# Kernel optimization log

Hardware: AMD Instinct MI355X
Metric: run time of the kernel (lower is better)

Reference implementation:

```python
import jax, jax.numpy as jnp
import numpy as np

F4_E2M1_MAX = 6.0
F8E4M3_MAX = 448.0
E4M3_EPS = 0.015625  # torch.finfo(float8_e4m3fn).tiny = 2**-6
BLOCK = 16
KE2M1 = jnp.array([0.0, 0.5, 1.0, 1.5, 2.0, 3.0, 4.0, 6.0], dtype=jnp.float32)


def round_to_e4m3(x):
    # emulate cast to float8_e4m3fn and back (round-to-nearest-even)
    return x.astype(jnp.float8_e4m3fn).astype(jnp.float32)


def fp4_121_positive(x):
    step1 = jnp.round(2.0 * x) / 2.0   # subnormal-ish region [0,2): step 0.5
    step2 = jnp.round(x)               # [2,4): step 1
    step3 = 2.0 * jnp.round(x / 2.0)   # [4,6]: step 2
    return jnp.where(x < 2.0, step1, jnp.where(x < 4.0, step2, step3))


def cast_to_fp4(x):
    return jnp.sign(x) * fp4_121_positive(jnp.abs(x))


def unpack_fp4_from_uint8(a, m, n):
    # a: int-typed tensor holding byte values in [0,256); two fp4 codes per byte
    high = (a.reshape(-1) >> 4) & 0xF
    low = a.reshape(-1) & 0xF
    combined = jnp.stack((low, high), axis=1).reshape(m, n)  # interleave low,high
    signs = (combined & 8) != 0
    abs_idx = combined & 7
    return KE2M1[abs_idx] * jnp.where(signs, -1.0, 1.0)


def dequant_nvfp4_packed(data_lp, out_scales, per_tensor_scale):
    m, half_n = data_lp.shape
    n = half_n * 2
    data_hp = unpack_fp4_from_uint8(data_lp, m, n)           # [m, n] float32
    scale_fp = out_scales / per_tensor_scale                  # [m, n/16]
    data_hp = data_hp.reshape(m, -1, BLOCK) * scale_fp.reshape(m, -1, 1)
    return data_hp.reshape(m, n)


def qdq_nvfp4(x):
    m, n = x.shape
    tensor_amax = jnp.max(jnp.abs(x))
    pts = jnp.clip(tensor_amax / F8E4M3_MAX, E4M3_EPS, F8E4M3_MAX)  # per-tensor scale
    xb = x.reshape(m, -1, BLOCK)
    block_scale = jnp.max(jnp.abs(xb), axis=-1) / F4_E2M1_MAX       # [m, n/16]
    scaled_bs = round_to_e4m3(jnp.clip(block_scale / pts, E4M3_EPS, F8E4M3_MAX))
    total_scale = pts * scaled_bs                                   # [m, n/16]
    data_scaled = jnp.clip(xb / total_scale[..., None], -F4_E2M1_MAX, F4_E2M1_MAX)
    data_lp = cast_to_fp4(data_scaled)                              # unpacked fp4 values
    # dequant: out_scales / (1/pts) == scaled_bs * pts == total_scale
    return (data_lp * total_scale[..., None]).reshape(m, n)


def setup_inputs() -> dict:
    key = jax.random.key(0)
    k1, k2, k3 = jax.random.split(key, 3)
    M, K, N = 16384, 2048, 2048  # tokens, in_features, out_features
    x = jax.random.normal(k1, (M, K), dtype=jnp.float32)
    weight_packed = jax.random.randint(k2, (N, K // 2), 0, 256, dtype=jnp.int32)
    # fp8-representable positive block scales
    weight_scale = round_to_e4m3(jax.random.uniform(k3, (N, K // 16), dtype=jnp.float32,
                                                    minval=0.05, maxval=1.0))
    weight_global_scale = jnp.ones((1,), dtype=jnp.float32)
    return {"x": x, "weight_packed": weight_packed,
            "weight_scale": weight_scale, "weight_global_scale": weight_global_scale}


def reference(x, weight_packed, weight_scale, weight_global_scale):
    hp_weight = dequant_nvfp4_packed(weight_packed, weight_scale, weight_global_scale)
    x_dq = qdq_nvfp4(x)
    return x_dq @ hp_weight.T
```

## Files before the change

kernel.cpp:

```cpp
#include <hip/hip_runtime.h>

typedef unsigned short u16;
typedef unsigned int u32;
typedef __attribute__((ext_vector_type(8))) short short8;
typedef __attribute__((ext_vector_type(4))) float floatx4;

static constexpr int M = 16384, N = 2048, K = 2048;


__device__ inline u16 f32_to_bf16(float x) {
    u32 u = __float_as_uint(x);
    u += 0x7FFFu + ((u >> 16) & 1u);
    return (u16)(u >> 16);
}

__device__ inline float e4m3_rne(float x) {
    u32 u = __float_as_uint(x);
    u += 0x7FFFFu + ((u >> 20) & 1u);
    u &= 0xFFF00000u;
    return __uint_as_float(u);
}

__device__ inline float fp4_dec(u32 c) {
    u32 e = (c >> 1) & 3u;
    float m = (float)(c & 1u);
    float v = e ? (2.0f + m) * (float)(1u << e) * 0.25f : 0.5f * m;
    return (c & 8u) ? -v : v;
}

__device__ inline float fp4_round_mag(float a) {
    if (a < 2.0f) return rintf(2.0f * a) * 0.5f;
    if (a < 4.0f) return rintf(a);
    return 2.0f * rintf(a * 0.5f);
}

__device__ inline float pts_from_amax(float amax) {
    return fminf(fmaxf(amax / 448.0f, 0.015625f), 448.0f);
}


__global__ void amax_kernel(const float4* __restrict__ x, u32* __restrict__ out, int n4) {
    int idx = blockIdx.x * blockDim.x + threadIdx.x;
    int stride = gridDim.x * blockDim.x;
    float m = 0.0f;
    for (int i = idx; i < n4; i += stride) {
        float4 v = x[i];
        m = fmaxf(m, fmaxf(fmaxf(fabsf(v.x), fabsf(v.y)), fmaxf(fabsf(v.z), fabsf(v.w))));
    }
#pragma unroll
    for (int off = 32; off > 0; off >>= 1)
        m = fmaxf(m, __shfl_down(m, off));
    __shared__ float sm[4];
    if ((threadIdx.x & 63) == 0) sm[threadIdx.x >> 6] = m;
    __syncthreads();
    if (threadIdx.x == 0) {
        m = fmaxf(fmaxf(sm[0], sm[1]), fmaxf(sm[2], sm[3]));
        atomicMax(out, __float_as_uint(m));
    }
}


__global__ void quant_x(const float* __restrict__ x, u16* __restrict__ aq,
                        const u32* __restrict__ amax_bits, int nblk) {
    int idx = blockIdx.x * blockDim.x + threadIdx.x;
    if (idx >= nblk) return;
    const float4* xp = (const float4*)(x + (size_t)idx * 16);
    float4 v[4];
#pragma unroll
    for (int i = 0; i < 4; i++) v[i] = xp[i];

    float bm = 0.0f;
#pragma unroll
    for (int i = 0; i < 4; i++)
        bm = fmaxf(bm, fmaxf(fmaxf(fabsf(v[i].x), fabsf(v[i].y)),
                             fmaxf(fabsf(v[i].z), fabsf(v[i].w))));

    float pts = pts_from_amax(__uint_as_float(*amax_bits));
    float bs = bm / 6.0f;
    float sbs = e4m3_rne(fminf(fmaxf(bs / pts, 0.015625f), 448.0f));
    float ts = pts * sbs;

    u16 o[16];
    const float* vf = (const float*)v;
#pragma unroll
    for (int i = 0; i < 16; i++) {
        float s = vf[i] / ts;
        s = fminf(fmaxf(s, -6.0f), 6.0f);
        float lp = copysignf(fp4_round_mag(fabsf(s)), s);
        o[i] = f32_to_bf16(lp * sbs);
    }
    uint4* op = (uint4*)(aq + (size_t)idx * 16);
    op[0] = ((const uint4*)o)[0];
    op[1] = ((const uint4*)o)[1];
}


__global__ void dequant_w(const int* __restrict__ wp, const float* __restrict__ wsc,
                          const float* __restrict__ wgs, u16* __restrict__ wq, int total) {
    int idx = blockIdx.x * blockDim.x + threadIdx.x;
    if (idx >= total) return;
    constexpr int Khalf = K / 2;
    int n = idx >> 10;
    int kb = idx & (Khalf - 1);
    u32 byte = (u32)wp[idx] & 0xFFu;
    float scale = wsc[(size_t)n * (K / 16) + (kb >> 3)] / wgs[0];
    float lo = fp4_dec(byte & 0xFu) * scale;
    float hi = fp4_dec((byte >> 4) & 0xFu) * scale;
    u32 out = (u32)f32_to_bf16(lo) | ((u32)f32_to_bf16(hi) << 16);
    ((u32*)wq)[idx] = out;
}


#define GLDS(g, l)                                                              \
    __builtin_amdgcn_global_load_lds(                                           \
        (const __attribute__((address_space(1))) unsigned int*)(g),             \
        (__attribute__((address_space(3))) unsigned int*)(l), 16, 0, 0)

__global__ __launch_bounds__(256, 3) void gemm_bt(
    const u16* __restrict__ A, const u16* __restrict__ B,
    float* __restrict__ C, const u32* __restrict__ amax_bits)
{
    __shared__ u16 lA[128 * 32];
    __shared__ u16 lB[128 * 32];

    const int tid = threadIdx.x;
    const int w = tid >> 6, lane = tid & 63;
    const int bm = blockIdx.x >> 4;
    const int bn = blockIdx.x & 15;
    const int wm = w >> 1, wn = w & 1;
    const int r = lane & 15, q = lane >> 4;

    floatx4 acc[4][4] = {};

    const int srow = lane >> 2;
    const int scol = (lane & 3) * 8;
    const u16* gA0 = A + (size_t)(bm * 128 + w * 32 + srow) * K + scol;
    const u16* gA1 = gA0 + (size_t)16 * K;
    const u16* gB0 = B + (size_t)(bn * 128 + w * 32 + srow) * K + scol;
    const u16* gB1 = gB0 + (size_t)16 * K;
    u16* lA0 = &lA[(w * 32) * 32];
    u16* lA1 = &lA[(w * 32 + 16) * 32];
    u16* lB0 = &lB[(w * 32) * 32];
    u16* lB1 = &lB[(w * 32 + 16) * 32];

    for (int kt = 0; kt < K; kt += 32) {
        GLDS(gA0 + kt, lA0);
        GLDS(gA1 + kt, lA1);
        GLDS(gB0 + kt, lB0);
        GLDS(gB1 + kt, lB1);
        __syncthreads();

        short8 af[4], bf[4];
#pragma unroll
        for (int i = 0; i < 4; i++)
            af[i] = *(const short8*)&lA[(wm * 64 + i * 16 + r) * 32 + q * 8];
#pragma unroll
        for (int j = 0; j < 4; j++)
            bf[j] = *(const short8*)&lB[(wn * 64 + j * 16 + r) * 32 + q * 8];

#pragma unroll
        for (int i = 0; i < 4; i++)
#pragma unroll
            for (int j = 0; j < 4; j++)
                acc[i][j] = __builtin_amdgcn_mfma_f32_16x16x32_bf16(
                    af[i], bf[j], acc[i][j], 0, 0, 0);

        __syncthreads();
    }

    float pts = pts_from_amax(__uint_as_float(*amax_bits));

    float* Cb = C + (size_t)(bm * 128 + wm * 64 + q * 4) * N + bn * 128 + wn * 64 + r;
#pragma unroll
    for (int i = 0; i < 4; i++)
#pragma unroll
        for (int j = 0; j < 4; j++)
#pragma unroll
            for (int t = 0; t < 4; t++)
                Cb[(size_t)(i * 16 + t) * N + j * 16] = pts * acc[i][j][t];
}


extern "C" void kernel_launch(void* const* d_in, const int* in_sizes, int n_in,
                              void* d_out, int out_size, void* d_ws, size_t ws_size,
                              hipStream_t stream) {
    const float* x   = (const float*)d_in[0];
    const int*   wp  = (const int*)d_in[1];
    const float* wsc = (const float*)d_in[2];
    const float* wgs = (const float*)d_in[3];
    float* out = (float*)d_out;

    u32* amax_ws = (u32*)d_ws;
    u16* aq = (u16*)((char*)d_ws + 256);
    u16* wq = aq + (size_t)M * K;

    hipMemsetAsync(d_ws, 0, 4, stream);
    amax_kernel<<<4096, 256, 0, stream>>>((const float4*)x, amax_ws, M * K / 4);
    quant_x<<<(M * K / 16) / 256, 256, 0, stream>>>(x, aq, amax_ws, M * K / 16);
    dequant_w<<<(N * (K / 2)) / 256, 256, 0, stream>>>(wp, wsc, wgs, wq, N * (K / 2));
    gemm_bt<<<(M / 128) * (N / 128), 256, 0, stream>>>(aq, wq, out, amax_ws);
}
```

Measured before the change: 436.0 us.

## Coalesce x quantization, two-stage amax reduction, XCD-aware GEMM tile mapping

Quantization of x now gives each thread one float4 instead of a full 16-element block, and combines the block max across 4 lanes with shuffles, so global loads and stores are coalesced. The amax reduction drops the memset and the global atomicMax in favour of per-block partial results plus a single-block final reduce, at the cost of one extra launch. The GEMM block index is remapped so that consecutive row tiles land on the same XCD, which is meant to improve L2 reuse of A across the N tiles.

```diff
diff --git a/kernel.cpp b/kernel.cpp
--- a/kernel.cpp
+++ b/kernel.cpp
@@ -39,7 +39,7 @@
 }
 
 
-__global__ void amax_kernel(const float4* __restrict__ x, u32* __restrict__ out, int n4) {
+__global__ void amax_part(const float4* __restrict__ x, float* __restrict__ part, int n4) {
     int idx = blockIdx.x * blockDim.x + threadIdx.x;
     int stride = gridDim.x * blockDim.x;
     float m = 0.0f;
@@ -53,45 +53,55 @@
     __shared__ float sm[4];
     if ((threadIdx.x & 63) == 0) sm[threadIdx.x >> 6] = m;
     __syncthreads();
-    if (threadIdx.x == 0) {
-        m = fmaxf(fmaxf(sm[0], sm[1]), fmaxf(sm[2], sm[3]));
-        atomicMax(out, __float_as_uint(m));
-    }
-}
-
-
-__global__ void quant_x(const float* __restrict__ x, u16* __restrict__ aq,
-                        const u32* __restrict__ amax_bits, int nblk) {
+    if (threadIdx.x == 0)
+        part[blockIdx.x] = fmaxf(fmaxf(sm[0], sm[1]), fmaxf(sm[2], sm[3]));
+}
+
+
+__global__ void amax_fin(const float* __restrict__ part, u32* __restrict__ out) {
+    int t = threadIdx.x;
+    float m = fmaxf(part[t], part[t + 1024]);
+#pragma unroll
+    for (int off = 32; off > 0; off >>= 1)
+        m = fmaxf(m, __shfl_down(m, off));
+    __shared__ float sm[16];
+    if ((t & 63) == 0) sm[t >> 6] = m;
+    __syncthreads();
+    if (t < 16) {
+        m = sm[t];
+#pragma unroll
+        for (int off = 8; off > 0; off >>= 1)
+            m = fmaxf(m, __shfl_down(m, off));
+        if (t == 0) *out = __float_as_uint(m);
+    }
+}
+
+
+__global__ void quant_x(const float4* __restrict__ x, uint2* __restrict__ aq,
+                        const u32* __restrict__ amax_bits, int nvec) {
     int idx = blockIdx.x * blockDim.x + threadIdx.x;
-    if (idx >= nblk) return;
-    const float4* xp = (const float4*)(x + (size_t)idx * 16);
-    float4 v[4];
-#pragma unroll
-    for (int i = 0; i < 4; i++) v[i] = xp[i];
-
-    float bm = 0.0f;
-#pragma unroll
-    for (int i = 0; i < 4; i++)
-        bm = fmaxf(bm, fmaxf(fmaxf(fabsf(v[i].x), fabsf(v[i].y)),
-                             fmaxf(fabsf(v[i].z), fabsf(v[i].w))));
+    if (idx >= nvec) return;
+    float4 v = x[idx];
+
+    float bm = fmaxf(fmaxf(fabsf(v.x), fabsf(v.y)), fmaxf(fabsf(v.z), fabsf(v.w)));
+    bm = fmaxf(bm, __shfl_xor(bm, 1));
+    bm = fmaxf(bm, __shfl_xor(bm, 2));
 
     float pts = pts_from_amax(__uint_as_float(*amax_bits));
     float bs = bm / 6.0f;
     float sbs = e4m3_rne(fminf(fmaxf(bs / pts, 0.015625f), 448.0f));
     float ts = pts * sbs;
 
-    u16 o[16];
-    const float* vf = (const float*)v;
-#pragma unroll
-    for (int i = 0; i < 16; i++) {
+    float vf[4] = {v.x, v.y, v.z, v.w};
+    u16 o[4];
+#pragma unroll
+    for (int i = 0; i < 4; i++) {
         float s = vf[i] / ts;
         s = fminf(fmaxf(s, -6.0f), 6.0f);
         float lp = copysignf(fp4_round_mag(fabsf(s)), s);
         o[i] = f32_to_bf16(lp * sbs);
     }
-    uint4* op = (uint4*)(aq + (size_t)idx * 16);
-    op[0] = ((const uint4*)o)[0];
-    op[1] = ((const uint4*)o)[1];
+    aq[idx] = *(const uint2*)o;
 }
 
 
@@ -125,8 +135,13 @@
 
     const int tid = threadIdx.x;
     const int w = tid >> 6, lane = tid & 63;
-    const int bm = blockIdx.x >> 4;
-    const int bn = blockIdx.x & 15;
+
+    const int id = blockIdx.x;
+    const int xcd = id & 7;
+    const int local = id >> 3;
+    const int bm = xcd * 16 + (local >> 4);
+    const int bn = local & 15;
+
     const int wm = w >> 1, wn = w & 1;
     const int r = lane & 15, q = lane >> 4;
 
@@ -190,13 +205,15 @@
     const float* wgs = (const float*)d_in[3];
     float* out = (float*)d_out;
 
-    u32* amax_ws = (u32*)d_ws;
-    u16* aq = (u16*)((char*)d_ws + 256);
-    u16* wq = aq + (size_t)M * K;
-
-    hipMemsetAsync(d_ws, 0, 4, stream);
-    amax_kernel<<<4096, 256, 0, stream>>>((const float4*)x, amax_ws, M * K / 4);
-    quant_x<<<(M * K / 16) / 256, 256, 0, stream>>>(x, aq, amax_ws, M * K / 16);
+    u32*   amax_ws = (u32*)d_ws;
+    float* part    = (float*)((char*)d_ws + 64);
+    u16*   aq      = (u16*)((char*)d_ws + 16384);
+    u16*   wq      = aq + (size_t)M * K;
+
+    amax_part<<<2048, 256, 0, stream>>>((const float4*)x, part, M * K / 4);
+    amax_fin<<<1, 1024, 0, stream>>>(part, amax_ws);
+    quant_x<<<(M * K / 4) / 256, 256, 0, stream>>>((const float4*)x, (uint2*)aq,
+                                                   amax_ws, M * K / 4);
     dequant_w<<<(N * (K / 2)) / 256, 256, 0, stream>>>(wp, wsc, wgs, wq, N * (K / 2));
     gemm_bt<<<(M / 128) * (N / 128), 256, 0, stream>>>(aq, wq, out, amax_ws);
 }
```

After: 413.2 us. -5.2%, faster.
